# Kernel optimization log

Hardware: AMD Instinct MI355X
Metric: run time of the kernel (lower is better)

The kernel has to match this reference:

```python
import jax, jax.numpy as jnp
import numpy as np

K = 9          # neighbors (module default k=9, dilation=1 -> plain top-k)
COUT = 256     # out_channels
BN_EPS = 1e-5


def setup_inputs() -> dict:
    key = jax.random.key(0)
    k1, k2 = jax.random.split(key, 2)
    x = jax.random.normal(k1, (8, 128, 2048, 1), jnp.float32)          # [B,C,N,1]
    W = jax.random.normal(k2, (COUT, 2 * 128), jnp.float32) * 0.05     # 1x1 conv weight [Cout, 2C]
    gamma = jnp.ones((COUT,), jnp.float32)                             # BN affine scale
    beta = jnp.zeros((COUT,), jnp.float32)                             # BN affine shift
    return {"x": x, "W": W, "gamma": gamma, "beta": beta}


def reference(x, W, gamma, beta):
    # x: [B, C, N, 1] channels-first point features
    xt = jnp.transpose(x[..., 0], (0, 2, 1))                           # [B, N, C]
    B, N, C = xt.shape

    # --- dense KNN graph (matrix form): squared euclidean distance, k nearest ---
    sq = jnp.sum(xt * xt, axis=-1)                                     # [B, N]
    dist = sq[:, :, None] - 2.0 * jnp.einsum('bnc,bmc->bnm', xt, xt) + sq[:, None, :]
    _, nn_idx = jax.lax.top_k(-dist, K)                                # [B, N, K] neighbor indices

    # --- EdgeConv gather: x_i = center, x_j = neighbor ---
    x_j = jax.vmap(lambda f, i: f[i])(xt, nn_idx)                      # [B, N, K, C]
    x_i = xt[:, :, None, :]                                            # [B, N, 1, C]
    feat = jnp.concatenate(
        [jnp.broadcast_to(x_i, (B, N, K, C)), x_j - x_i], axis=-1)     # [B, N, K, 2C]

    # --- 1x1 conv (no bias) as GEMM over channel dim ---
    h = jnp.einsum('bnkc,oc->bnko', feat, W)                           # [B, N, K, Cout]

    # --- BatchNorm2d (training-mode batch stats over B,N,K per channel) ---
    mean = jnp.mean(h, axis=(0, 1, 2))
    var = jnp.var(h, axis=(0, 1, 2))
    hn = (h - mean) * jax.lax.rsqrt(var + BN_EPS) * gamma + beta

    # --- ReLU then max over k neighbors ---
    out = jnp.max(jax.nn.relu(hn), axis=2)                             # [B, N, Cout]
    return jnp.transpose(out, (0, 2, 1))                               # [B, Cout, N]
```

## Files before the change

kernel.cpp:

```cpp
#include <hip/hip_runtime.h>
#include <float.h>
#include <math.h>

#define BATCH 8
#define CHN   128
#define NPTS  2048
#define KNN   9
#define NOUT  256
#define TOTCNT (BATCH*NPTS*KNN)

typedef __attribute__((ext_vector_type(8))) short short8;
typedef __attribute__((ext_vector_type(4))) float f32x4;

__device__ __forceinline__ unsigned short f2bf(float f) {
    unsigned int u = __float_as_uint(f);
    unsigned int r = (u + 0x7FFFu + ((u >> 16) & 1u)) >> 16;
    return (unsigned short)r;
}
__device__ __forceinline__ float bf2f(unsigned short h) {
    return __uint_as_float(((unsigned int)h) << 16);
}

__global__ __launch_bounds__(256) void prep_kernel(const float* __restrict__ x,
                                                   unsigned short* __restrict__ xhi,
                                                   unsigned short* __restrict__ xlo,
                                                   float* __restrict__ sqh) {
    __shared__ float xt[128 * 65];
    __shared__ float psq[256];
    const int b = blockIdx.x, n0 = blockIdx.y * 64, tid = threadIdx.x;
#pragma unroll 4
    for (int p = 0; p < 32; ++p) {
        int c = p * 4 + (tid >> 6), n = tid & 63;
        xt[c * 65 + n] = x[((size_t)b * CHN + c) * NPTS + n0 + n];
    }
    __syncthreads();
    const int n = tid >> 2, cq = tid & 3;
    size_t row = (size_t)(b * NPTS + n0 + n) * CHN;
    float s = 0.f;
#pragma unroll 8
    for (int j = 0; j < 32; ++j) {
        int c = cq * 32 + j;
        float f = xt[c * 65 + n];
        unsigned short h = f2bf(f);
        float hf = bf2f(h);
        unsigned short l = f2bf(f - hf);
        xhi[row + c] = h;
        xlo[row + c] = l;
        s += f * f;
    }
    psq[tid] = s;
    __syncthreads();
    if (tid < 64)
        sqh[b * NPTS + n0 + tid] =
            0.5f * (psq[tid*4] + psq[tid*4+1] + psq[tid*4+2] + psq[tid*4+3]);
}

__global__ __launch_bounds__(256) void wprep_kernel(const float* __restrict__ W,
                                                    unsigned short* __restrict__ whi,
                                                    unsigned short* __restrict__ wlo) {
    int t = blockIdx.x * 256 + threadIdx.x;
    int r = t >> 5, c0 = (t & 31) * 4;
#pragma unroll
    for (int e = 0; e < 4; ++e) {
        int c = c0 + e;
        float v = (r < 256) ? (W[r * 256 + c] - W[r * 256 + 128 + c])
                            : W[(r - 256) * 256 + 128 + c];
        unsigned short h = f2bf(v);
        float hf = bf2f(h);
        unsigned short l = f2bf(v - hf);
        whi[r * 128 + c] = h;
        wlo[r * 128 + c] = l;
    }
}

__global__ __launch_bounds__(256) void knn_mfma(const unsigned short* __restrict__ xhi,
                                                const unsigned short* __restrict__ xlo,
                                                const float* __restrict__ sqh,
                                                float* __restrict__ pd,
                                                int* __restrict__ pi) {
    __shared__ __align__(16) float dts[64 * 132];

    const int tid = threadIdx.x;
    const int b = blockIdx.x, q0 = blockIdx.y * 64, ms = blockIdx.z;
    const int msbase = ms * 512;
    const int wv = tid >> 6, lane = tid & 63;
    const int quad = lane >> 4, col = lane & 15;
    const int koff = quad * 8;
    const int mcol0 = wv * 32;
    const size_t xb = (size_t)b * NPTS * CHN;

    float dl[KNN]; int il[KNN];
#pragma unroll
    for (int k = 0; k < KNN; ++k) { dl[k] = FLT_MAX; il[k] = 0; }

    const int qsc = tid >> 2, ss = tid & 3;
    const int cb = ss * 32;

    auto ins = [&](float v, int idx) {
        if (v < dl[KNN - 1]) {
            bool c0b = v < dl[0];
#pragma unroll
            for (int k = KNN - 1; k >= 1; --k) {
                bool sh   = v < dl[k - 1];
                bool here = v < dl[k];
                float nd = sh ? dl[k - 1] : (here ? v : dl[k]);
                int   ni = sh ? il[k - 1] : (here ? idx : il[k]);
                dl[k] = nd; il[k] = ni;
            }
            if (c0b) { dl[0] = v; il[0] = idx; }
        }
    };

    for (int iter = 0; iter < 4; ++iter) {
        const int mbase = msbase + iter * 128;
        float sm[2];
#pragma unroll
        for (int j = 0; j < 2; ++j)
            sm[j] = sqh[b * NPTS + mbase + mcol0 + j * 16 + col];

        f32x4 acc[4][2];
#pragma unroll
        for (int i = 0; i < 4; ++i)
#pragma unroll
            for (int j = 0; j < 2; ++j) acc[i][j] = (f32x4)0.f;

        for (int chk = 0; chk < 4; ++chk) {
            short8 ah[4], al[4];
#pragma unroll
            for (int i = 0; i < 4; ++i) {
                size_t g = xb + (size_t)(q0 + i * 16 + col) * CHN + chk * 32 + koff;
                ah[i] = *(const short8*)&xhi[g];
                al[i] = *(const short8*)&xlo[g];
            }
#pragma unroll
            for (int j = 0; j < 2; ++j) {
                size_t g = xb + (size_t)(mbase + mcol0 + j * 16 + col) * CHN + chk * 32 + koff;
                short8 bh = *(const short8*)&xhi[g];
                short8 bl = *(const short8*)&xlo[g];
#pragma unroll
                for (int i = 0; i < 4; ++i) {
                    acc[i][j] = __builtin_amdgcn_mfma_f32_16x16x32_bf16(ah[i], bh, acc[i][j], 0, 0, 0);
                    acc[i][j] = __builtin_amdgcn_mfma_f32_16x16x32_bf16(ah[i], bl, acc[i][j], 0, 0, 0);
                    acc[i][j] = __builtin_amdgcn_mfma_f32_16x16x32_bf16(al[i], bh, acc[i][j], 0, 0, 0);
                }
            }
        }

        __syncthreads();
#pragma unroll
        for (int j = 0; j < 2; ++j)
#pragma unroll
            for (int i = 0; i < 4; ++i)
#pragma unroll
                for (int r = 0; r < 4; ++r) {
                    int q_ = i * 16 + quad * 4 + r;
                    dts[q_ * 132 + mcol0 + j * 16 + col] = sm[j] - acc[i][j][r];
                }
        __syncthreads();
        const int ibase = mbase + cb;
#pragma unroll
        for (int jj = 0; jj < 8; ++jj) {
            float4 v = *(const float4*)&dts[qsc * 132 + cb + jj * 4];
            float mn4 = fminf(fminf(v.x, v.y), fminf(v.z, v.w));
            if (mn4 < dl[KNN - 1]) {
                int ib = ibase + jj * 4;
                ins(v.x, ib); ins(v.y, ib + 1); ins(v.z, ib + 2); ins(v.w, ib + 3);
            }
        }
    }

    __syncthreads();
    float* md = dts;
    int*   mi = (int*)(dts + 2304);
#pragma unroll
    for (int k = 0; k < KNN; ++k) {
        md[qsc * 36 + ss * 9 + k] = dl[k];
        mi[qsc * 36 + ss * 9 + k] = il[k];
    }
    __syncthreads();
    if (tid < 64) {
        int base = tid * 36;
        int p0 = 0, p1 = 0, p2 = 0, p3 = 0;
        size_t ob = ((size_t)(b * NPTS + q0 + tid) * 4 + ms) * KNN;
        for (int k = 0; k < KNN; ++k) {
            float v0 = (p0 < KNN) ? md[base + p0]      : FLT_MAX;
            float v1 = (p1 < KNN) ? md[base + 9 + p1]  : FLT_MAX;
            float v2 = (p2 < KNN) ? md[base + 18 + p2] : FLT_MAX;
            float v3 = (p3 < KNN) ? md[base + 27 + p3] : FLT_MAX;
            float best = v0; int sel = 0;
            if (v1 < best) { best = v1; sel = 1; }
            if (v2 < best) { best = v2; sel = 2; }
            if (v3 < best) { best = v3; sel = 3; }
            int idx;
            if      (sel == 0) { idx = mi[base + p0];      p0++; }
            else if (sel == 1) { idx = mi[base + 9 + p1];  p1++; }
            else if (sel == 2) { idx = mi[base + 18 + p2]; p2++; }
            else               { idx = mi[base + 27 + p3]; p3++; }
            pd[ob + k] = best;
            pi[ob + k] = idx;
        }
    }
}

__global__ __launch_bounds__(256) void merge4_kernel(const float* __restrict__ pd,
                                                     const int* __restrict__ pi,
                                                     int* __restrict__ nn) {
    int q = blockIdx.x * 256 + threadIdx.x;
    const float* d = pd + (size_t)q * 36;
    const int*   i = pi + (size_t)q * 36;
    int p0 = 0, p1 = 0, p2 = 0, p3 = 0;
#pragma unroll
    for (int k = 0; k < KNN; ++k) {
        float v0 = (p0 < KNN) ? d[p0]      : FLT_MAX;
        float v1 = (p1 < KNN) ? d[9 + p1]  : FLT_MAX;
        float v2 = (p2 < KNN) ? d[18 + p2] : FLT_MAX;
        float v3 = (p3 < KNN) ? d[27 + p3] : FLT_MAX;
        float best = v0; int sel = 0;
        if (v1 < best) { best = v1; sel = 1; }
        if (v2 < best) { best = v2; sel = 2; }
        if (v3 < best) { best = v3; sel = 3; }
        int idx;
        if      (sel == 0) { idx = i[p0];      p0++; }
        else if (sel == 1) { idx = i[9 + p1];  p1++; }
        else if (sel == 2) { idx = i[18 + p2]; p2++; }
        else               { idx = i[27 + p3]; p3++; }
        nn[q * KNN + k] = idx;
    }
}

__global__ __launch_bounds__(256) void pq_mfma(const unsigned short* __restrict__ xhi,
                                               const unsigned short* __restrict__ xlo,
                                               const unsigned short* __restrict__ whi,
                                               const unsigned short* __restrict__ wlo,
                                               float* __restrict__ p,
                                               float* __restrict__ q) {
    const int tid = threadIdx.x;
    const int b = blockIdx.x, nt = blockIdx.y, ot = blockIdx.z;
    const int wv = tid >> 6, lane = tid & 63;
    const int quad = lane >> 4, col = lane & 15;
    const int koff = quad * 8;
    const size_t xb = (size_t)b * NPTS * CHN;
    const int nbase = nt * 256 + wv * 64;
    const int obase = ot * 64;

    f32x4 acc[4][4];
#pragma unroll
    for (int i = 0; i < 4; ++i)
#pragma unroll
        for (int j = 0; j < 4; ++j) acc[i][j] = (f32x4)0.f;

    for (int chk = 0; chk < 4; ++chk) {
        short8 ah[4], al[4];
#pragma unroll
        for (int i = 0; i < 4; ++i) {
            size_t g = xb + (size_t)(nbase + i * 16 + col) * CHN + chk * 32 + koff;
            ah[i] = *(const short8*)&xhi[g];
            al[i] = *(const short8*)&xlo[g];
        }
#pragma unroll
        for (int j = 0; j < 4; ++j) {
            size_t g = (size_t)(obase + j * 16 + col) * CHN + chk * 32 + koff;
            short8 bh = *(const short8*)&whi[g];
            short8 bl = *(const short8*)&wlo[g];
#pragma unroll
            for (int i = 0; i < 4; ++i) {
                acc[i][j] = __builtin_amdgcn_mfma_f32_16x16x32_bf16(ah[i], bh, acc[i][j], 0, 0, 0);
                acc[i][j] = __builtin_amdgcn_mfma_f32_16x16x32_bf16(ah[i], bl, acc[i][j], 0, 0, 0);
                acc[i][j] = __builtin_amdgcn_mfma_f32_16x16x32_bf16(al[i], bh, acc[i][j], 0, 0, 0);
            }
        }
    }
    float* dst = (ot < 4) ? p : q;
#pragma unroll
    for (int i = 0; i < 4; ++i)
#pragma unroll
        for (int j = 0; j < 4; ++j) {
            int oc = (obase + j * 16 + col) & 255;
#pragma unroll
            for (int r = 0; r < 4; ++r) {
                int n = nbase + i * 16 + quad * 4 + r;
                dst[(size_t)(b * NPTS + n) * NOUT + oc] = acc[i][j][r];
            }
        }
}

__global__ __launch_bounds__(256) void stats2_kernel(float* __restrict__ p,
                                                     const float* __restrict__ q,
                                                     const int* __restrict__ nn,
                                                     float* __restrict__ stats,
                                                     float* __restrict__ hmn) {
    __shared__ int idx_s[32 * KNN];
    const int b = blockIdx.x, n0 = blockIdx.y * 32;
    const int o = threadIdx.x;
    for (int t = threadIdx.x; t < 32 * KNN; t += 256)
        idx_s[t] = nn[(size_t)(b * NPTS + n0) * KNN + t];
    __syncthreads();
    const float* qb = q + (size_t)b * NPTS * NOUT + o;
    float s = 0.f, ss = 0.f;
    for (int qq = 0; qq < 32; ++qq) {
        size_t off = (size_t)(b * NPTS + n0 + qq) * NOUT + o;
        float pv = p[off];
        float h[KNN];
#pragma unroll
        for (int k = 0; k < KNN; ++k)
            h[k] = pv + qb[(size_t)idx_s[qq * KNN + k] * NOUT];
        float mx = h[0], mn = h[0];
#pragma unroll
        for (int k = 0; k < KNN; ++k) {
            s += h[k]; ss += h[k] * h[k];
            mx = fmaxf(mx, h[k]); mn = fminf(mn, h[k]);
        }
        p[off] = mx;
        hmn[off] = mn;
    }
    atomicAdd(&stats[o], s);
    atomicAdd(&stats[NOUT + o], ss);
}

__global__ __launch_bounds__(256) void final_kernel(const float* __restrict__ hmx,
                                                    const float* __restrict__ hmn,
                                                    const float* __restrict__ stats,
                                                    const float* __restrict__ gamma,
                                                    const float* __restrict__ beta,
                                                    float* __restrict__ out) {
    __shared__ float tr[256 * 17];
    const int b = blockIdx.x, n0 = blockIdx.y * 16;
    const int o = threadIdx.x;
    const float inv = 1.f / (float)TOTCNT;
    float mean = stats[o] * inv;
    float var  = stats[NOUT + o] * inv - mean * mean;
    float g    = gamma[o] / sqrtf(var + 1e-5f);
    float bet  = beta[o];
    for (int qq = 0; qq < 16; ++qq) {
        size_t off = (size_t)(b * NPTS + n0 + qq) * NOUT + o;
        float v = (g >= 0.f) ? hmx[off] : hmn[off];
        float hn = (v - mean) * g + bet;
        tr[o * 17 + qq] = fmaxf(hn, 0.f);
    }
    __syncthreads();
    int oo = threadIdx.x >> 4, qq = threadIdx.x & 15;
    for (int pass = 0; pass < 16; ++pass) {
        int o_ = pass * 16 + oo;
        out[((size_t)b * NOUT + o_) * NPTS + n0 + qq] = tr[o_ * 17 + qq];
    }
}

extern "C" void kernel_launch(void* const* d_in, const int* in_sizes, int n_in,
                              void* d_out, int out_size, void* d_ws, size_t ws_size,
                              hipStream_t stream) {
    (void)in_sizes; (void)n_in; (void)out_size; (void)ws_size;
    const float* x     = (const float*)d_in[0];
    const float* W     = (const float*)d_in[1];
    const float* gamma = (const float*)d_in[2];
    const float* beta  = (const float*)d_in[3];
    float* out = (float*)d_out;

    char* ws = (char*)d_ws;
    float*          p     = (float*)ws;
    float*          q     = (float*)(ws + (16u << 20));
    unsigned short* xhi   = (unsigned short*)(ws + (32u << 20));
    unsigned short* xlo   = (unsigned short*)(ws + (36u << 20));
    float*          pd    = (float*)(ws + (40u << 20));
    int*            pi    = (int*)  (ws + (43u << 20));
    unsigned short* whi   = (unsigned short*)(ws + (46u << 20));
    unsigned short* wlo   = (unsigned short*)(ws + (46u << 20) + 131072);
    float*          hmn   = (float*)(ws + (32u << 20));
    float*          sqh   = (float*)(ws + (48u << 20));
    float*          stats = (float*)(ws + (48u << 20) + 65536);
    int*            nn    = (int*)  (ws + (48u << 20) + 65536 + 4096);

    hipMemsetAsync(stats, 0, 2 * NOUT * sizeof(float), stream);
    wprep_kernel <<<64,             256, 0, stream>>>(W, whi, wlo);
    prep_kernel  <<<dim3(8, 32),    256, 0, stream>>>(x, xhi, xlo, sqh);
    knn_mfma     <<<dim3(8, 32, 4), 256, 0, stream>>>(xhi, xlo, sqh, pd, pi);
    merge4_kernel<<<64,             256, 0, stream>>>(pd, pi, nn);
    pq_mfma      <<<dim3(8, 8, 8),  256, 0, stream>>>(xhi, xlo, whi, wlo, p, q);
    stats2_kernel<<<dim3(8, 64),    256, 0, stream>>>(p, q, nn, stats, hmn);
    final_kernel <<<dim3(8, 128),   256, 0, stream>>>(p, hmn, stats, gamma, beta, out);
}
```

Measured before the change: 224.9 us.

## Give each wave its own query rows to drop block-wide barriers in KNN

```diff
diff --git a/kernel.cpp b/kernel.cpp
--- a/kernel.cpp
+++ b/kernel.cpp
@@ -78,22 +78,22 @@
                                                 const float* __restrict__ sqh,
                                                 float* __restrict__ pd,
                                                 int* __restrict__ pi) {
-    __shared__ __align__(16) float dts[64 * 132];
+    __shared__ __align__(16) float dts[4][16 * 132];
 
     const int tid = threadIdx.x;
     const int b = blockIdx.x, q0 = blockIdx.y * 64, ms = blockIdx.z;
-    const int msbase = ms * 512;
     const int wv = tid >> 6, lane = tid & 63;
     const int quad = lane >> 4, col = lane & 15;
     const int koff = quad * 8;
-    const int mcol0 = wv * 32;
+    const int qw = q0 + wv * 16;
     const size_t xb = (size_t)b * NPTS * CHN;
+    float* dtw = &dts[wv][0];
 
     float dl[KNN]; int il[KNN];
 #pragma unroll
     for (int k = 0; k < KNN; ++k) { dl[k] = FLT_MAX; il[k] = 0; }
 
-    const int qsc = tid >> 2, ss = tid & 3;
+    const int qsc = lane >> 2, ss = lane & 3;
     const int cb = ss * 32;
 
     auto ins = [&](float v, int idx) {
@@ -111,56 +111,44 @@
         }
     };
 
+    const size_t ga0 = xb + (size_t)(qw + col) * CHN + koff;
+
     for (int iter = 0; iter < 4; ++iter) {
-        const int mbase = msbase + iter * 128;
-        float sm[2];
-#pragma unroll
-        for (int j = 0; j < 2; ++j)
-            sm[j] = sqh[b * NPTS + mbase + mcol0 + j * 16 + col];
-
-        f32x4 acc[4][2];
-#pragma unroll
-        for (int i = 0; i < 4; ++i)
-#pragma unroll
-            for (int j = 0; j < 2; ++j) acc[i][j] = (f32x4)0.f;
+        const int mbase = ms * 512 + iter * 128;
+        float sm[8];
+#pragma unroll
+        for (int j = 0; j < 8; ++j)
+            sm[j] = sqh[b * NPTS + mbase + j * 16 + col];
+
+        f32x4 acc[8];
+#pragma unroll
+        for (int j = 0; j < 8; ++j) acc[j] = (f32x4)0.f;
 
         for (int chk = 0; chk < 4; ++chk) {
-            short8 ah[4], al[4];
-#pragma unroll
-            for (int i = 0; i < 4; ++i) {
-                size_t g = xb + (size_t)(q0 + i * 16 + col) * CHN + chk * 32 + koff;
-                ah[i] = *(const short8*)&xhi[g];
-                al[i] = *(const short8*)&xlo[g];
-            }
-#pragma unroll
-            for (int j = 0; j < 2; ++j) {
-                size_t g = xb + (size_t)(mbase + mcol0 + j * 16 + col) * CHN + chk * 32 + koff;
-                short8 bh = *(const short8*)&xhi[g];
-                short8 bl = *(const short8*)&xlo[g];
-#pragma unroll
-                for (int i = 0; i < 4; ++i) {
-                    acc[i][j] = __builtin_amdgcn_mfma_f32_16x16x32_bf16(ah[i], bh, acc[i][j], 0, 0, 0);
-                    acc[i][j] = __builtin_amdgcn_mfma_f32_16x16x32_bf16(ah[i], bl, acc[i][j], 0, 0, 0);
-                    acc[i][j] = __builtin_amdgcn_mfma_f32_16x16x32_bf16(al[i], bh, acc[i][j], 0, 0, 0);
-                }
-            }
-        }
-
-        __syncthreads();
-#pragma unroll
-        for (int j = 0; j < 2; ++j)
-#pragma unroll
-            for (int i = 0; i < 4; ++i)
-#pragma unroll
-                for (int r = 0; r < 4; ++r) {
-                    int q_ = i * 16 + quad * 4 + r;
-                    dts[q_ * 132 + mcol0 + j * 16 + col] = sm[j] - acc[i][j][r];
-                }
-        __syncthreads();
+            short8 ah = *(const short8*)&xhi[ga0 + chk * 32];
+            short8 al = *(const short8*)&xlo[ga0 + chk * 32];
+#pragma unroll
+            for (int j = 0; j < 8; ++j) {
+                size_t gb = xb + (size_t)(mbase + j * 16 + col) * CHN + chk * 32 + koff;
+                short8 bh = *(const short8*)&xhi[gb];
+                short8 bl = *(const short8*)&xlo[gb];
+                acc[j] = __builtin_amdgcn_mfma_f32_16x16x32_bf16(ah, bh, acc[j], 0, 0, 0);
+                acc[j] = __builtin_amdgcn_mfma_f32_16x16x32_bf16(ah, bl, acc[j], 0, 0, 0);
+                acc[j] = __builtin_amdgcn_mfma_f32_16x16x32_bf16(al, bh, acc[j], 0, 0, 0);
+            }
+        }
+
+#pragma unroll
+        for (int j = 0; j < 8; ++j)
+#pragma unroll
+            for (int r = 0; r < 4; ++r) {
+                int q_ = quad * 4 + r;
+                dtw[q_ * 132 + j * 16 + col] = sm[j] - acc[j][r];
+            }
         const int ibase = mbase + cb;
 #pragma unroll
         for (int jj = 0; jj < 8; ++jj) {
-            float4 v = *(const float4*)&dts[qsc * 132 + cb + jj * 4];
+            float4 v = *(const float4*)&dtw[qsc * 132 + cb + jj * 4];
             float mn4 = fminf(fminf(v.x, v.y), fminf(v.z, v.w));
             if (mn4 < dl[KNN - 1]) {
                 int ib = ibase + jj * 4;
@@ -169,19 +157,17 @@
         }
     }
 
-    __syncthreads();
-    float* md = dts;
-    int*   mi = (int*)(dts + 2304);
+    float* md = dtw;
+    int*   mi = (int*)(dtw + 16 * 36);
 #pragma unroll
     for (int k = 0; k < KNN; ++k) {
         md[qsc * 36 + ss * 9 + k] = dl[k];
         mi[qsc * 36 + ss * 9 + k] = il[k];
     }
-    __syncthreads();
-    if (tid < 64) {
-        int base = tid * 36;
+    if (lane < 16) {
+        int base = lane * 36;
         int p0 = 0, p1 = 0, p2 = 0, p3 = 0;
-        size_t ob = ((size_t)(b * NPTS + q0 + tid) * 4 + ms) * KNN;
+        size_t ob = ((size_t)(b * NPTS + qw + lane) * 4 + ms) * KNN;
         for (int k = 0; k < KNN; ++k) {
             float v0 = (p0 < KNN) ? md[base + p0]      : FLT_MAX;
             float v1 = (p1 < KNN) ? md[base + 9 + p1]  : FLT_MAX;
```

After: 285.6 us. 27.0% more time.
